# Kernel optimization log

Hardware: AMD Instinct MI355X
Metric: run time of the kernel (lower is better)

## Reference

```python
import jax, jax.numpy as jnp
import numpy as np

BLOCK_LEN = 64

def _segsum(x):
    """x: (..., T) -> (..., T, T) with segment sums on/below diagonal, -inf above."""
    T = x.shape[-1]
    cs = jnp.cumsum(x, axis=-1)
    seg = cs[..., :, None] - cs[..., None, :]
    mask = jnp.tril(jnp.ones((T, T), dtype=bool))
    return jnp.where(mask, seg, -jnp.inf)

def setup_inputs() -> dict:
    key = jax.random.key(0)
    kX, kA, kB, kC = jax.random.split(key, 4)
    B, S, H, P, N = 2, 4096, 32, 64, 64
    X = jax.random.normal(kX, (B, S, H, P), dtype=jnp.float32)
    # negative decay rates keep exp(cumsum) bounded (real Mamba2 uses A<0)
    A = -jnp.abs(jax.random.normal(kA, (B, S, H), dtype=jnp.float32)) * 0.1
    Bm = jax.random.normal(kB, (B, S, H, N), dtype=jnp.float32)
    Cm = jax.random.normal(kC, (B, S, H, N), dtype=jnp.float32)
    return {"X": X, "A": A, "Bm": Bm, "Cm": Cm}

def reference(X, A, Bm, Cm):
    b, s, h, p = X.shape
    n = Bm.shape[-1]
    l = BLOCK_LEN
    c = s // l
    Xb = X.reshape(b, c, l, h, p)
    Bb = Bm.reshape(b, c, l, h, n)
    Cb = Cm.reshape(b, c, l, h, n)
    Ab = A.reshape(b, c, l, h).transpose(0, 3, 1, 2)  # (b,h,c,l)

    # intra-chunk decay matrix L = exp(segsum(A))  (b,h,c,l,l)
    L = jnp.exp(_segsum(Ab))
    Y_diag = jnp.einsum('bclhn,bcshn,bhcls,bcshp->bclhp', Cb, Bb, L, Xb)

    A_cumsum = jnp.cumsum(Ab, axis=-1)  # (b,h,c,l)
    decay_states = jnp.exp(A_cumsum[..., :, -1:] - A_cumsum)
    states = jnp.einsum('bclhn,bhcl,bclhp->bchpn', Bb, decay_states, Xb)

    init = jnp.zeros_like(states[:, :1])
    states = jnp.concatenate([init, states], axis=1)  # (b,c+1,h,p,n)

    chunk_last = jnp.pad(A_cumsum[..., -1], ((0, 0), (0, 0), (1, 0)))  # (b,h,c+1)
    decay_chunk = jnp.exp(_segsum(chunk_last))  # (b,h,c+1,c+1)
    new_states = jnp.einsum('bhzc,bchpn->bzhpn', decay_chunk, states)
    states = new_states[:, :-1]  # (b,c,h,p,n)

    state_decay_out = jnp.exp(A_cumsum)
    Y_off = jnp.einsum('bclhn,bchpn,bhcl->bclhp', Cb, states, state_decay_out)

    Y = (Y_diag + Y_off).reshape(b, s, h, p)
    return Y
```

## Files before the change

kernel.cpp:

```cpp
#include <hip/hip_runtime.h>

#define B_ 2
#define S_ 4096
#define H_ 32
#define P_ 64
#define N_ 64
#define C_ 64
#define HP 2048
#define HN 2048

typedef __attribute__((ext_vector_type(8))) short bf16x8;
typedef __attribute__((ext_vector_type(4))) float f32x4;

__device__ __forceinline__ float bf2f(unsigned int u16) {
    return __uint_as_float(u16 << 16);
}
__device__ __forceinline__ void unpack2(unsigned int u, float& lo, float& hi) {
    lo = __uint_as_float(u << 16);
    hi = __uint_as_float(u & 0xffff0000u);
}
__device__ __forceinline__ unsigned short f2bf(float f) {
    unsigned int u = __float_as_uint(f);
    u += 0x7fffu + ((u >> 16) & 1u);
    return (unsigned short)(u >> 16);
}
__device__ __forceinline__ void split_bf(float x, unsigned short& h, unsigned short& l) {
    h = f2bf(x);
    l = f2bf(x - bf2f(h));
}

__device__ __forceinline__ int nsw(int r, int cb) {
    return (r << 7) + (cb ^ ((r & 7) << 4));
}
__device__ __forceinline__ int tsw(int r, int cb) {
    return (r << 7) + (cb ^ ((((r & 7) ^ (r >> 3)) & 7) << 4));
}

__global__ void k0_detect(const unsigned short* __restrict__ Au, int* __restrict__ flag)
{
    int tid = threadIdx.x;
    unsigned short u = Au[tid * 2];
    int positive = ((u & 0x8000u) == 0) ? 1 : 0;
    unsigned long long m = __ballot(positive);
    if (tid == 0) *flag = (__popcll(m) > 8) ? 1 : 0;
}

__global__ __launch_bounds__(256, 4) void k1u(
    const void* __restrict__ Xg,
    const void* __restrict__ Ag,
    const void* __restrict__ Bg,
    float* __restrict__ states,
    float* __restrict__ sums,
    const int* __restrict__ flag)
{
    __shared__ __align__(16) unsigned short XTh[4096];
    __shared__ __align__(16) unsigned short XTl[4096];
    __shared__ __align__(16) unsigned short BTh[4096];
    __shared__ __align__(16) unsigned short BTl[4096];
    __shared__ float wdec[64];

    const int tid = threadIdx.x;
    const int bid = blockIdx.x;
    const int h = bid & 31, c = (bid >> 5) & 63, b = bid >> 11;
    const int isf32 = *flag;

    if (tid < 64) {
        int ai = (b * S_ + c * 64 + tid) * H_ + h;
        float a = isf32 ? ((const float*)Ag)[ai] : bf2f(((const unsigned short*)Ag)[ai]);
        float x = a;
        #pragma unroll
        for (int off = 1; off < 64; off <<= 1) {
            float y = __shfl_up(x, off, 64);
            if (tid >= off) x += y;
        }
        float tot = __shfl(x, 63, 64);
        wdec[tid] = __expf(tot - x);
        if (tid == 63) sums[(b * H_ + h) * C_ + c] = tot;
    }
    __syncthreads();

    const size_t baseX = (size_t)((b * S_ + c * 64) * H_ + h) * P_;
    const size_t baseB = (size_t)((b * S_ + c * 64) * H_ + h) * N_;
    char* XThb = (char*)XTh;
    char* XTlb = (char*)XTl;
    char* BThb = (char*)BTh;
    char* BTlb = (char*)BTl;

    #pragma unroll
    for (int it = 0; it < 2; ++it) {
        int t = (tid >> 3) + it * 32;
        int e = (tid & 7) * 8;
        float xv[8], bv[8];
        if (isf32) {
            const float* Xp = (const float*)Xg + baseX + (size_t)t * HP + e;
            const float* Bp = (const float*)Bg + baseB + (size_t)t * HN + e;
            float4 x0 = *(const float4*)Xp;
            float4 x1 = *(const float4*)(Xp + 4);
            float4 b0 = *(const float4*)Bp;
            float4 b1 = *(const float4*)(Bp + 4);
            xv[0]=x0.x; xv[1]=x0.y; xv[2]=x0.z; xv[3]=x0.w;
            xv[4]=x1.x; xv[5]=x1.y; xv[6]=x1.z; xv[7]=x1.w;
            bv[0]=b0.x; bv[1]=b0.y; bv[2]=b0.z; bv[3]=b0.w;
            bv[4]=b1.x; bv[5]=b1.y; bv[6]=b1.z; bv[7]=b1.w;
        } else {
            const unsigned short* Xp = (const unsigned short*)Xg + baseX + (size_t)t * HP + e;
            const unsigned short* Bp = (const unsigned short*)Bg + baseB + (size_t)t * HN + e;
            uint4 rx = *(const uint4*)Xp;
            uint4 rb = *(const uint4*)Bp;
            unpack2(rx.x, xv[0], xv[1]); unpack2(rx.y, xv[2], xv[3]);
            unpack2(rx.z, xv[4], xv[5]); unpack2(rx.w, xv[6], xv[7]);
            unpack2(rb.x, bv[0], bv[1]); unpack2(rb.y, bv[2], bv[3]);
            unpack2(rb.z, bv[4], bv[5]); unpack2(rb.w, bv[6], bv[7]);
        }
        float w = wdec[t];
        #pragma unroll
        for (int i = 0; i < 8; ++i) {
            int o = tsw(e + i, 2 * t);
            unsigned short hh, ll;
            split_bf(xv[i], hh, ll);
            *(unsigned short*)(XThb + o) = hh;
            *(unsigned short*)(XTlb + o) = ll;
            split_bf(bv[i] * w, hh, ll);
            *(unsigned short*)(BThb + o) = hh;
            *(unsigned short*)(BTlb + o) = ll;
        }
    }
    __syncthreads();

    const int l = tid & 63, w4 = tid >> 6;
    const int lr = l & 15, q = l >> 4;
    const int rowA = 16 * w4 + lr;

    const int oa0 = tsw(rowA, 16 * q);
    const int oa1 = tsw(rowA, 16 * q + 64);
    bf16x8 a0h = *(const bf16x8*)(XThb + oa0);
    bf16x8 a1h = *(const bf16x8*)(XThb + oa1);
    bf16x8 a0l = *(const bf16x8*)(XTlb + oa0);
    bf16x8 a1l = *(const bf16x8*)(XTlb + oa1);

    f32x4 acc[4];
    #pragma unroll
    for (int nt = 0; nt < 4; ++nt) acc[nt] = (f32x4){0.f, 0.f, 0.f, 0.f};
    #pragma unroll
    for (int nt = 0; nt < 4; ++nt) {
        int ob0 = tsw(16 * nt + lr, 16 * q);
        int ob1 = tsw(16 * nt + lr, 16 * q + 64);
        bf16x8 b0h = *(const bf16x8*)(BThb + ob0);
        bf16x8 b0l = *(const bf16x8*)(BTlb + ob0);
        bf16x8 b1h = *(const bf16x8*)(BThb + ob1);
        bf16x8 b1l = *(const bf16x8*)(BTlb + ob1);
        acc[nt] = __builtin_amdgcn_mfma_f32_16x16x32_bf16(a0h, b0h, acc[nt], 0, 0, 0);
        acc[nt] = __builtin_amdgcn_mfma_f32_16x16x32_bf16(a1h, b1h, acc[nt], 0, 0, 0);
        acc[nt] = __builtin_amdgcn_mfma_f32_16x16x32_bf16(a0h, b0l, acc[nt], 0, 0, 0);
        acc[nt] = __builtin_amdgcn_mfma_f32_16x16x32_bf16(a1h, b1l, acc[nt], 0, 0, 0);
        acc[nt] = __builtin_amdgcn_mfma_f32_16x16x32_bf16(a0l, b0h, acc[nt], 0, 0, 0);
        acc[nt] = __builtin_amdgcn_mfma_f32_16x16x32_bf16(a1l, b1h, acc[nt], 0, 0, 0);
    }

    float* sp = states + (size_t)((b * C_ + c) * H_ + h) * 4096;
    #pragma unroll
    for (int nt = 0; nt < 4; ++nt)
        #pragma unroll
        for (int r = 0; r < 4; ++r) {
            int p = 16 * w4 + 4 * q + r;
            int n = 16 * nt + lr;
            sp[p * 64 + n] = acc[nt][r];
        }
}

__global__ __launch_bounds__(256) void k2_scan(
    float* __restrict__ states, const float* __restrict__ sums)
{
    const int tid = threadIdx.x;
    const int bid = blockIdx.x;
    const int split = bid & 7;
    const int bh = bid >> 3;
    const int h = bh & 31;
    const int b = bh >> 5;
    const int e = split * 512 + tid * 2;
    const float* sm = sums + (b * H_ + h) * C_;
    const size_t cstride = (size_t)H_ * 4096;
    float* p = states + ((size_t)(b * C_) * H_ + h) * 4096 + e;
    float2 S = make_float2(0.f, 0.f);
    float2 st = *(const float2*)p;
    #pragma unroll 4
    for (int c = 0; c < 64; ++c) {
        float2 stn = make_float2(0.f, 0.f);
        if (c < 63) stn = *(const float2*)(p + cstride);
        float d = __expf(sm[c]);
        *(float2*)p = S;
        S.x = S.x * d + st.x;
        S.y = S.y * d + st.y;
        st = stn;
        p += cstride;
    }
}

__global__ __launch_bounds__(256, 3) void k3u(
    const void* __restrict__ Xg,
    const void* __restrict__ Ag,
    const void* __restrict__ Bg,
    const void* __restrict__ Cg,
    const float* __restrict__ states,
    void* __restrict__ Yg,
    const int* __restrict__ flag)
{
    __shared__ __align__(16) unsigned short Ch[4096];
    __shared__ __align__(16) unsigned short Cl[4096];
    __shared__ __align__(16) unsigned short Bh[4096];
    __shared__ __align__(16) unsigned short Bl[4096];
    __shared__ __align__(16) unsigned short Sh[4096];
    __shared__ __align__(16) unsigned short Sl[4096];
    __shared__ float csh[64];

    const int tid = threadIdx.x;
    const int bid = blockIdx.x;
    const int h = bid & 31, c = (bid >> 5) & 63, b = bid >> 11;
    const int isf32 = *flag;

    if (tid < 64) {
        int ai = (b * S_ + c * 64 + tid) * H_ + h;
        float a = isf32 ? ((const float*)Ag)[ai] : bf2f(((const unsigned short*)Ag)[ai]);
        float x = a;
        #pragma unroll
        for (int off = 1; off < 64; off <<= 1) {
            float y = __shfl_up(x, off, 64);
            if (tid >= off) x += y;
        }
        csh[tid] = x;
    }

    const size_t baseX = (size_t)((b * S_ + c * 64) * H_ + h) * P_;
    const size_t baseN = (size_t)((b * S_ + c * 64) * H_ + h) * N_;
    char* Chb = (char*)Ch; char* Clb = (char*)Cl;
    char* Bhb = (char*)Bh; char* Blb = (char*)Bl;
    char* Shb = (char*)Sh; char* Slb = (char*)Sl;

    uint4 xq0[2], xq1[2];
    #pragma unroll
    for (int it = 0; it < 2; ++it) {
        int t = (tid >> 3) + it * 32;
        int e = (tid & 7) * 8;
        if (isf32) {
            const float* Xp = (const float*)Xg + baseX + (size_t)t * HP + e;
            xq0[it] = *(const uint4*)Xp;
            xq1[it] = *(const uint4*)(Xp + 4);
        } else {
            const unsigned short* Xp = (const unsigned short*)Xg + baseX + (size_t)t * HP + e;
            xq0[it] = *(const uint4*)Xp;
        }
    }

    #pragma unroll
    for (int it = 0; it < 2; ++it) {
        int t = (tid >> 3) + it * 32;
        int e = (tid & 7) * 8;
        float cv[8], bv[8];
        if (isf32) {
            const float* Cp = (const float*)Cg + baseN + (size_t)t * HN + e;
            const float* Bp = (const float*)Bg + baseN + (size_t)t * HN + e;
            float4 c0 = *(const float4*)Cp;
            float4 c1 = *(const float4*)(Cp + 4);
            float4 b0 = *(const float4*)Bp;
            float4 b1 = *(const float4*)(Bp + 4);
            cv[0]=c0.x; cv[1]=c0.y; cv[2]=c0.z; cv[3]=c0.w;
            cv[4]=c1.x; cv[5]=c1.y; cv[6]=c1.z; cv[7]=c1.w;
            bv[0]=b0.x; bv[1]=b0.y; bv[2]=b0.z; bv[3]=b0.w;
            bv[4]=b1.x; bv[5]=b1.y; bv[6]=b1.z; bv[7]=b1.w;
        } else {
            const unsigned short* Cp = (const unsigned short*)Cg + baseN + (size_t)t * HN + e;
            const unsigned short* Bp = (const unsigned short*)Bg + baseN + (size_t)t * HN + e;
            uint4 rc = *(const uint4*)Cp;
            uint4 rb = *(const uint4*)Bp;
            unpack2(rc.x, cv[0], cv[1]); unpack2(rc.y, cv[2], cv[3]);
            unpack2(rc.z, cv[4], cv[5]); unpack2(rc.w, cv[6], cv[7]);
            unpack2(rb.x, bv[0], bv[1]); unpack2(rb.y, bv[2], bv[3]);
            unpack2(rb.z, bv[4], bv[5]); unpack2(rb.w, bv[6], bv[7]);
        }
        int o = nsw(t, 2 * e);
        unsigned short hs[8], ls[8];
        #pragma unroll
        for (int i = 0; i < 8; ++i) split_bf(cv[i], hs[i], ls[i]);
        {
            uint4 uh, ul;
            uh.x = (unsigned int)hs[0] | ((unsigned int)hs[1] << 16);
            uh.y = (unsigned int)hs[2] | ((unsigned int)hs[3] << 16);
            uh.z = (unsigned int)hs[4] | ((unsigned int)hs[5] << 16);
            uh.w = (unsigned int)hs[6] | ((unsigned int)hs[7] << 16);
            ul.x = (unsigned int)ls[0] | ((unsigned int)ls[1] << 16);
            ul.y = (unsigned int)ls[2] | ((unsigned int)ls[3] << 16);
            ul.z = (unsigned int)ls[4] | ((unsigned int)ls[5] << 16);
            ul.w = (unsigned int)ls[6] | ((unsigned int)ls[7] << 16);
            *(uint4*)(Chb + o) = uh;
            *(uint4*)(Clb + o) = ul;
        }
        #pragma unroll
        for (int i = 0; i < 8; ++i) split_bf(bv[i], hs[i], ls[i]);
        {
            uint4 uh, ul;
            uh.x = (unsigned int)hs[0] | ((unsigned int)hs[1] << 16);
            uh.y = (unsigned int)hs[2] | ((unsigned int)hs[3] << 16);
            uh.z = (unsigned int)hs[4] | ((unsigned int)hs[5] << 16);
            uh.w = (unsigned int)hs[6] | ((unsigned int)hs[7] << 16);
            ul.x = (unsigned int)ls[0] | ((unsigned int)ls[1] << 16);
            ul.y = (unsigned int)ls[2] | ((unsigned int)ls[3] << 16);
            ul.z = (unsigned int)ls[4] | ((unsigned int)ls[5] << 16);
            ul.w = (unsigned int)ls[6] | ((unsigned int)ls[7] << 16);
            *(uint4*)(Bhb + o) = uh;
            *(uint4*)(Blb + o) = ul;
        }
    }

    {
        const float* sb = states + (size_t)((b * C_ + c) * H_ + h) * 4096;
        #pragma unroll
        for (int k = 0; k < 4; ++k) {
            int e2 = (k * 256 + tid) * 4;
            float4 v = *(const float4*)(sb + e2);
            unsigned short h0,l0,h1,l1,h2,l2,h3,l3;
            split_bf(v.x, h0, l0); split_bf(v.y, h1, l1);
            split_bf(v.z, h2, l2); split_bf(v.w, h3, l3);
            uint2 uh, ul;
            uh.x = (unsigned int)h0 | ((unsigned int)h1 << 16);
            uh.y = (unsigned int)h2 | ((unsigned int)h3 << 16);
            ul.x = (unsigned int)l0 | ((unsigned int)l1 << 16);
            ul.y = (unsigned int)l2 | ((unsigned int)l3 << 16);
            int o = nsw(e2 >> 6, 2 * (e2 & 63));
            *(uint2*)(Shb + o) = uh;
            *(uint2*)(Slb + o) = ul;
        }
    }
    __syncthreads();

    const int l = tid & 63, w4 = tid >> 6;
    const int lr = l & 15, q = l >> 4;
    const int tA = 16 * w4 + lr;

    const int oa0 = nsw(tA, 16 * q);
    const int oa1 = nsw(tA, 16 * q + 64);
    bf16x8 ac0h = *(const bf16x8*)(Chb + oa0);
    bf16x8 ac1h = *(const bf16x8*)(Chb + oa1);
    bf16x8 ac0l = *(const bf16x8*)(Clb + oa0);
    bf16x8 ac1l = *(const bf16x8*)(Clb + oa1);

    f32x4 mac[4];
    #pragma unroll
    for (int st = 0; st < 4; ++st) mac[st] = (f32x4){0.f, 0.f, 0.f, 0.f};
    #pragma unroll
    for (int st = 0; st < 4; ++st) {
        int ob0 = nsw(16 * st + lr, 16 * q);
        int ob1 = nsw(16 * st + lr, 16 * q + 64);
        bf16x8 b0h = *(const bf16x8*)(Bhb + ob0);
        bf16x8 b0l = *(const bf16x8*)(Blb + ob0);
        bf16x8 b1h = *(const bf16x8*)(Bhb + ob1);
        bf16x8 b1l = *(const bf16x8*)(Blb + ob1);
        mac[st] = __builtin_amdgcn_mfma_f32_16x16x32_bf16(ac0h, b0h, mac[st], 0, 0, 0);
        mac[st] = __builtin_amdgcn_mfma_f32_16x16x32_bf16(ac1h, b1h, mac[st], 0, 0, 0);
        mac[st] = __builtin_amdgcn_mfma_f32_16x16x32_bf16(ac0h, b0l, mac[st], 0, 0, 0);
        mac[st] = __builtin_amdgcn_mfma_f32_16x16x32_bf16(ac1h, b1l, mac[st], 0, 0, 0);
        mac[st] = __builtin_amdgcn_mfma_f32_16x16x32_bf16(ac0l, b0h, mac[st], 0, 0, 0);
        mac[st] = __builtin_amdgcn_mfma_f32_16x16x32_bf16(ac1l, b1h, mac[st], 0, 0, 0);
    }

    f32x4 yacO[4];
    #pragma unroll
    for (int pt = 0; pt < 4; ++pt) yacO[pt] = (f32x4){0.f, 0.f, 0.f, 0.f};
    #pragma unroll
    for (int pt = 0; pt < 4; ++pt) {
        int os0 = nsw(16 * pt + lr, 16 * q);
        int os1 = nsw(16 * pt + lr, 16 * q + 64);
        bf16x8 s0h = *(const bf16x8*)(Shb + os0);
        bf16x8 s0l = *(const bf16x8*)(Slb + os0);
        bf16x8 s1h = *(const bf16x8*)(Shb + os1);
        bf16x8 s1l = *(const bf16x8*)(Slb + os1);
        yacO[pt] = __builtin_amdgcn_mfma_f32_16x16x32_bf16(ac0h, s0h, yacO[pt], 0, 0, 0);
        yacO[pt] = __builtin_amdgcn_mfma_f32_16x16x32_bf16(ac1h, s1h, yacO[pt], 0, 0, 0);
        yacO[pt] = __builtin_amdgcn_mfma_f32_16x16x32_bf16(ac0h, s0l, yacO[pt], 0, 0, 0);
        yacO[pt] = __builtin_amdgcn_mfma_f32_16x16x32_bf16(ac1h, s1l, yacO[pt], 0, 0, 0);
        yacO[pt] = __builtin_amdgcn_mfma_f32_16x16x32_bf16(ac0l, s0h, yacO[pt], 0, 0, 0);
        yacO[pt] = __builtin_amdgcn_mfma_f32_16x16x32_bf16(ac1l, s1h, yacO[pt], 0, 0, 0);
    }
    __syncthreads();

    float ct[4];
    #pragma unroll
    for (int r = 0; r < 4; ++r) ct[r] = csh[16 * w4 + 4 * q + r];
    #pragma unroll
    for (int st = 0; st < 4; ++st) {
        int s = 16 * st + lr;
        float cs_s = csh[s];
        #pragma unroll
        for (int r = 0; r < 4; ++r) {
            int t = 16 * w4 + 4 * q + r;
            float v = (s <= t) ? mac[st][r] * __expf(ct[r] - cs_s) : 0.f;
            unsigned short hh, ll;
            split_bf(v, hh, ll);
            int o = nsw(t, 2 * s);
            *(unsigned short*)(Bhb + o) = hh;
            *(unsigned short*)(Blb + o) = ll;
        }
    }

    #pragma unroll
    for (int it = 0; it < 2; ++it) {
        int t = (tid >> 3) + it * 32;
        int e = (tid & 7) * 8;
        float xv[8];
        if (isf32) {
            xv[0] = __uint_as_float(xq0[it].x); xv[1] = __uint_as_float(xq0[it].y);
            xv[2] = __uint_as_float(xq0[it].z); xv[3] = __uint_as_float(xq0[it].w);
            xv[4] = __uint_as_float(xq1[it].x); xv[5] = __uint_as_float(xq1[it].y);
            xv[6] = __uint_as_float(xq1[it].z); xv[7] = __uint_as_float(xq1[it].w);
        } else {
            unpack2(xq0[it].x, xv[0], xv[1]); unpack2(xq0[it].y, xv[2], xv[3]);
            unpack2(xq0[it].z, xv[4], xv[5]); unpack2(xq0[it].w, xv[6], xv[7]);
        }
        #pragma unroll
        for (int i = 0; i < 8; ++i) {
            unsigned short hh, ll;
            split_bf(xv[i], hh, ll);
            int o = tsw(e + i, 2 * t);
            *(unsigned short*)(Shb + o) = hh;
            *(unsigned short*)(Slb + o) = ll;
        }
    }
    __syncthreads();

    const int om0 = nsw(tA, 16 * q);
    const int om1 = nsw(tA, 16 * q + 64);
    bf16x8 am0h = *(const bf16x8*)(Bhb + om0);
    bf16x8 am1h = *(const bf16x8*)(Bhb + om1);
    bf16x8 am0l = *(const bf16x8*)(Blb + om0);
    bf16x8 am1l = *(const bf16x8*)(Blb + om1);
    f32x4 yacD[4];
    #pragma unroll
    for (int pt = 0; pt < 4; ++pt) yacD[pt] = (f32x4){0.f, 0.f, 0.f, 0.f};
    #pragma unroll
    for (int pt = 0; pt < 4; ++pt) {
        int ox0 = tsw(16 * pt + lr, 16 * q);
        int ox1 = tsw(16 * pt + lr, 16 * q + 64);
        bf16x8 x0h = *(const bf16x8*)(Shb + ox0);
        bf16x8 x0l = *(const bf16x8*)(Slb + ox0);
        bf16x8 x1h = *(const bf16x8*)(Shb + ox1);
        bf16x8 x1l = *(const bf16x8*)(Slb + ox1);
        yacD[pt] = __builtin_amdgcn_mfma_f32_16x16x32_bf16(am0h, x0h, yacD[pt], 0, 0, 0);
        yacD[pt] = __builtin_amdgcn_mfma_f32_16x16x32_bf16(am1h, x1h, yacD[pt], 0, 0, 0);
        yacD[pt] = __builtin_amdgcn_mfma_f32_16x16x32_bf16(am0h, x0l, yacD[pt], 0, 0, 0);
        yacD[pt] = __builtin_amdgcn_mfma_f32_16x16x32_bf16(am1h, x1l, yacD[pt], 0, 0, 0);
        yacD[pt] = __builtin_amdgcn_mfma_f32_16x16x32_bf16(am0l, x0h, yacD[pt], 0, 0, 0);
        yacD[pt] = __builtin_amdgcn_mfma_f32_16x16x32_bf16(am1l, x1h, yacD[pt], 0, 0, 0);
    }

    float ge[4];
    #pragma unroll
    for (int r = 0; r < 4; ++r) ge[r] = __expf(ct[r]);
    if (!isf32) {
        unsigned short* Yp = (unsigned short*)Yg + baseX;
        #pragma unroll
        for (int pt = 0; pt < 4; ++pt)
            #pragma unroll
            for (int r = 0; r < 4; ++r) {
                int t = 16 * w4 + 4 * q + r;
                Yp[(size_t)t * HP + 16 * pt + lr] = f2bf(yacD[pt][r] + ge[r] * yacO[pt][r]);
            }
    } else {
        float* Yp = (float*)Yg + baseX;
        #pragma unroll
        for (int pt = 0; pt < 4; ++pt)
            #pragma unroll
            for (int r = 0; r < 4; ++r) {
                int t = 16 * w4 + 4 * q + r;
                Yp[(size_t)t * HP + 16 * pt + lr] = yacD[pt][r] + ge[r] * yacO[pt][r];
            }
    }
}

extern "C" void kernel_launch(void* const* d_in, const int* in_sizes, int n_in,
                              void* d_out, int out_size, void* d_ws, size_t ws_size,
                              hipStream_t stream) {
    const void* X  = d_in[0];
    const void* A  = d_in[1];
    const void* Bm = d_in[2];
    const void* Cm = d_in[3];

    int*   flag   = (int*)d_ws;
    float* sums   = (float*)d_ws + 16;
    float* states = (float*)d_ws + 16 + 4096;

    k0_detect<<<dim3(1), dim3(64), 0, stream>>>((const unsigned short*)A, flag);
    k1u<<<dim3(B_ * C_ * H_), dim3(256), 0, stream>>>(X, A, Bm, states, sums, flag);
    k2_scan<<<dim3(B_ * H_ * 8), dim3(256), 0, stream>>>(states, sums);
    k3u<<<dim3(B_ * C_ * H_), dim3(256), 0, stream>>>(X, A, Bm, Cm, states, d_out, flag);
}
```

Measured before the change: 282.6 us.

## Fuse detect, chunk-state, scan and output kernels into one cooperative persistent kernel

Replaces the four separate launches (dtype detect, per-chunk state GEMM, inter-chunk scan, output GEMM) with one cooperative kernel. Persistent blocks loop over tiles and are separated by grid-wide syncs. Loads are issued earlier so they overlap the decay scan, and the scan stage caches the per-chunk exp decays in shared memory and prefetches several chunks ahead. The aim is to remove launch gaps and per-kernel ramp costs. In exchange it adds grid.sync overhead and depends on the assumed count of 256 CUs and the occupancy query to size the grid.

```diff
diff --git a/kernel.cpp b/kernel.cpp
--- a/kernel.cpp
+++ b/kernel.cpp
@@ -1,4 +1,7 @@
 #include <hip/hip_runtime.h>
+#include <hip/hip_cooperative_groups.h>
+
+namespace cg = cooperative_groups;
 
 #define B_ 2
 #define S_ 4096
@@ -8,6 +11,7 @@
 #define C_ 64
 #define HP 2048
 #define HN 2048
+#define NTILE 4096
 
 typedef __attribute__((ext_vector_type(8))) short bf16x8;
 typedef __attribute__((ext_vector_type(4))) float f32x4;
@@ -36,459 +40,468 @@
     return (r << 7) + (cb ^ ((((r & 7) ^ (r >> 3)) & 7) << 4));
 }
 
-__global__ void k0_detect(const unsigned short* __restrict__ Au, int* __restrict__ flag)
-{
-    int tid = threadIdx.x;
-    unsigned short u = Au[tid * 2];
-    int positive = ((u & 0x8000u) == 0) ? 1 : 0;
-    unsigned long long m = __ballot(positive);
-    if (tid == 0) *flag = (__popcll(m) > 8) ? 1 : 0;
-}
-
-__global__ __launch_bounds__(256, 4) void k1u(
-    const void* __restrict__ Xg,
-    const void* __restrict__ Ag,
-    const void* __restrict__ Bg,
-    float* __restrict__ states,
-    float* __restrict__ sums,
-    const int* __restrict__ flag)
-{
-    __shared__ __align__(16) unsigned short XTh[4096];
-    __shared__ __align__(16) unsigned short XTl[4096];
-    __shared__ __align__(16) unsigned short BTh[4096];
-    __shared__ __align__(16) unsigned short BTl[4096];
-    __shared__ float wdec[64];
-
-    const int tid = threadIdx.x;
-    const int bid = blockIdx.x;
-    const int h = bid & 31, c = (bid >> 5) & 63, b = bid >> 11;
-    const int isf32 = *flag;
-
-    if (tid < 64) {
-        int ai = (b * S_ + c * 64 + tid) * H_ + h;
-        float a = isf32 ? ((const float*)Ag)[ai] : bf2f(((const unsigned short*)Ag)[ai]);
-        float x = a;
-        #pragma unroll
-        for (int off = 1; off < 64; off <<= 1) {
-            float y = __shfl_up(x, off, 64);
-            if (tid >= off) x += y;
-        }
-        float tot = __shfl(x, 63, 64);
-        wdec[tid] = __expf(tot - x);
-        if (tid == 63) sums[(b * H_ + h) * C_ + c] = tot;
-    }
-    __syncthreads();
-
-    const size_t baseX = (size_t)((b * S_ + c * 64) * H_ + h) * P_;
-    const size_t baseB = (size_t)((b * S_ + c * 64) * H_ + h) * N_;
-    char* XThb = (char*)XTh;
-    char* XTlb = (char*)XTl;
-    char* BThb = (char*)BTh;
-    char* BTlb = (char*)BTl;
-
-    #pragma unroll
-    for (int it = 0; it < 2; ++it) {
-        int t = (tid >> 3) + it * 32;
-        int e = (tid & 7) * 8;
-        float xv[8], bv[8];
-        if (isf32) {
-            const float* Xp = (const float*)Xg + baseX + (size_t)t * HP + e;
-            const float* Bp = (const float*)Bg + baseB + (size_t)t * HN + e;
-            float4 x0 = *(const float4*)Xp;
-            float4 x1 = *(const float4*)(Xp + 4);
-            float4 b0 = *(const float4*)Bp;
-            float4 b1 = *(const float4*)(Bp + 4);
-            xv[0]=x0.x; xv[1]=x0.y; xv[2]=x0.z; xv[3]=x0.w;
-            xv[4]=x1.x; xv[5]=x1.y; xv[6]=x1.z; xv[7]=x1.w;
-            bv[0]=b0.x; bv[1]=b0.y; bv[2]=b0.z; bv[3]=b0.w;
-            bv[4]=b1.x; bv[5]=b1.y; bv[6]=b1.z; bv[7]=b1.w;
-        } else {
-            const unsigned short* Xp = (const unsigned short*)Xg + baseX + (size_t)t * HP + e;
-            const unsigned short* Bp = (const unsigned short*)Bg + baseB + (size_t)t * HN + e;
-            uint4 rx = *(const uint4*)Xp;
-            uint4 rb = *(const uint4*)Bp;
-            unpack2(rx.x, xv[0], xv[1]); unpack2(rx.y, xv[2], xv[3]);
-            unpack2(rx.z, xv[4], xv[5]); unpack2(rx.w, xv[6], xv[7]);
-            unpack2(rb.x, bv[0], bv[1]); unpack2(rb.y, bv[2], bv[3]);
-            unpack2(rb.z, bv[4], bv[5]); unpack2(rb.w, bv[6], bv[7]);
-        }
-        float w = wdec[t];
-        #pragma unroll
-        for (int i = 0; i < 8; ++i) {
-            int o = tsw(e + i, 2 * t);
-            unsigned short hh, ll;
-            split_bf(xv[i], hh, ll);
-            *(unsigned short*)(XThb + o) = hh;
-            *(unsigned short*)(XTlb + o) = ll;
-            split_bf(bv[i] * w, hh, ll);
-            *(unsigned short*)(BThb + o) = hh;
-            *(unsigned short*)(BTlb + o) = ll;
-        }
-    }
-    __syncthreads();
-
-    const int l = tid & 63, w4 = tid >> 6;
-    const int lr = l & 15, q = l >> 4;
-    const int rowA = 16 * w4 + lr;
-
-    const int oa0 = tsw(rowA, 16 * q);
-    const int oa1 = tsw(rowA, 16 * q + 64);
-    bf16x8 a0h = *(const bf16x8*)(XThb + oa0);
-    bf16x8 a1h = *(const bf16x8*)(XThb + oa1);
-    bf16x8 a0l = *(const bf16x8*)(XTlb + oa0);
-    bf16x8 a1l = *(const bf16x8*)(XTlb + oa1);
-
-    f32x4 acc[4];
-    #pragma unroll
-    for (int nt = 0; nt < 4; ++nt) acc[nt] = (f32x4){0.f, 0.f, 0.f, 0.f};
-    #pragma unroll
-    for (int nt = 0; nt < 4; ++nt) {
-        int ob0 = tsw(16 * nt + lr, 16 * q);
-        int ob1 = tsw(16 * nt + lr, 16 * q + 64);
-        bf16x8 b0h = *(const bf16x8*)(BThb + ob0);
-        bf16x8 b0l = *(const bf16x8*)(BTlb + ob0);
-        bf16x8 b1h = *(const bf16x8*)(BThb + ob1);
-        bf16x8 b1l = *(const bf16x8*)(BTlb + ob1);
-        acc[nt] = __builtin_amdgcn_mfma_f32_16x16x32_bf16(a0h, b0h, acc[nt], 0, 0, 0);
-        acc[nt] = __builtin_amdgcn_mfma_f32_16x16x32_bf16(a1h, b1h, acc[nt], 0, 0, 0);
-        acc[nt] = __builtin_amdgcn_mfma_f32_16x16x32_bf16(a0h, b0l, acc[nt], 0, 0, 0);
-        acc[nt] = __builtin_amdgcn_mfma_f32_16x16x32_bf16(a1h, b1l, acc[nt], 0, 0, 0);
-        acc[nt] = __builtin_amdgcn_mfma_f32_16x16x32_bf16(a0l, b0h, acc[nt], 0, 0, 0);
-        acc[nt] = __builtin_amdgcn_mfma_f32_16x16x32_bf16(a1l, b1h, acc[nt], 0, 0, 0);
-    }
-
-    float* sp = states + (size_t)((b * C_ + c) * H_ + h) * 4096;
-    #pragma unroll
-    for (int nt = 0; nt < 4; ++nt)
-        #pragma unroll
-        for (int r = 0; r < 4; ++r) {
-            int p = 16 * w4 + 4 * q + r;
-            int n = 16 * nt + lr;
-            sp[p * 64 + n] = acc[nt][r];
-        }
-}
-
-__global__ __launch_bounds__(256) void k2_scan(
-    float* __restrict__ states, const float* __restrict__ sums)
-{
-    const int tid = threadIdx.x;
-    const int bid = blockIdx.x;
-    const int split = bid & 7;
-    const int bh = bid >> 3;
-    const int h = bh & 31;
-    const int b = bh >> 5;
-    const int e = split * 512 + tid * 2;
-    const float* sm = sums + (b * H_ + h) * C_;
-    const size_t cstride = (size_t)H_ * 4096;
-    float* p = states + ((size_t)(b * C_) * H_ + h) * 4096 + e;
-    float2 S = make_float2(0.f, 0.f);
-    float2 st = *(const float2*)p;
-    #pragma unroll 4
-    for (int c = 0; c < 64; ++c) {
-        float2 stn = make_float2(0.f, 0.f);
-        if (c < 63) stn = *(const float2*)(p + cstride);
-        float d = __expf(sm[c]);
-        *(float2*)p = S;
-        S.x = S.x * d + st.x;
-        S.y = S.y * d + st.y;
-        st = stn;
-        p += cstride;
-    }
-}
-
-__global__ __launch_bounds__(256, 3) void k3u(
+__global__ __launch_bounds__(256, 3) void fused(
     const void* __restrict__ Xg,
     const void* __restrict__ Ag,
     const void* __restrict__ Bg,
     const void* __restrict__ Cg,
-    const float* __restrict__ states,
-    void* __restrict__ Yg,
-    const int* __restrict__ flag)
+    float* __restrict__ states,
+    float* __restrict__ sums,
+    void* __restrict__ Yg)
 {
-    __shared__ __align__(16) unsigned short Ch[4096];
-    __shared__ __align__(16) unsigned short Cl[4096];
-    __shared__ __align__(16) unsigned short Bh[4096];
-    __shared__ __align__(16) unsigned short Bl[4096];
-    __shared__ __align__(16) unsigned short Sh[4096];
-    __shared__ __align__(16) unsigned short Sl[4096];
-    __shared__ float csh[64];
-
-    const int tid = threadIdx.x;
-    const int bid = blockIdx.x;
-    const int h = bid & 31, c = (bid >> 5) & 63, b = bid >> 11;
-    const int isf32 = *flag;
-
-    if (tid < 64) {
-        int ai = (b * S_ + c * 64 + tid) * H_ + h;
-        float a = isf32 ? ((const float*)Ag)[ai] : bf2f(((const unsigned short*)Ag)[ai]);
-        float x = a;
-        #pragma unroll
-        for (int off = 1; off < 64; off <<= 1) {
-            float y = __shfl_up(x, off, 64);
-            if (tid >= off) x += y;
-        }
-        csh[tid] = x;
+    __shared__ __align__(16) unsigned char pool[49408];
+    char*  p0  = (char*)pool;
+    float* fsh = (float*)(pool + 49152);
+
+    const int tid  = threadIdx.x;
+    const int nblk = gridDim.x;
+    cg::grid_group grid = cg::this_grid();
+
+    int isf32;
+    {
+        unsigned short du = ((const unsigned short*)Ag)[(tid & 63) * 2];
+        unsigned long long m = __ballot(((du & 0x8000u) == 0) ? 1 : 0);
+        isf32 = (__popcll(m) > 8) ? 1 : 0;
     }
 
-    const size_t baseX = (size_t)((b * S_ + c * 64) * H_ + h) * P_;
-    const size_t baseN = (size_t)((b * S_ + c * 64) * H_ + h) * N_;
-    char* Chb = (char*)Ch; char* Clb = (char*)Cl;
-    char* Bhb = (char*)Bh; char* Blb = (char*)Bl;
-    char* Shb = (char*)Sh; char* Slb = (char*)Sl;
-
-    uint4 xq0[2], xq1[2];
-    #pragma unroll
-    for (int it = 0; it < 2; ++it) {
-        int t = (tid >> 3) + it * 32;
-        int e = (tid & 7) * 8;
-        if (isf32) {
-            const float* Xp = (const float*)Xg + baseX + (size_t)t * HP + e;
-            xq0[it] = *(const uint4*)Xp;
-            xq1[it] = *(const uint4*)(Xp + 4);
-        } else {
-            const unsigned short* Xp = (const unsigned short*)Xg + baseX + (size_t)t * HP + e;
-            xq0[it] = *(const uint4*)Xp;
-        }
+    const int l  = tid & 63, w4 = tid >> 6;
+    const int lr = l & 15,  q  = l >> 4;
+
+    for (int tile = blockIdx.x; tile < NTILE; tile += nblk) {
+        const int h = tile & 31, c = (tile >> 5) & 63, b = tile >> 11;
+        char* XThb = p0;
+        char* XTlb = p0 + 8192;
+        char* BThb = p0 + 16384;
+        char* BTlb = p0 + 24576;
+        float* wdec = fsh;
+
+        const size_t baseX = (size_t)((b * S_ + c * 64) * H_ + h) * P_;
+        const size_t baseB = (size_t)((b * S_ + c * 64) * H_ + h) * N_;
+
+        uint4 xA[2], xB[2], bA[2], bB[2];
+        #pragma unroll
+        for (int it = 0; it < 2; ++it) {
+            int t = (tid >> 3) + it * 32;
+            int e = (tid & 7) * 8;
+            if (isf32) {
+                const float* Xp = (const float*)Xg + baseX + (size_t)t * HP + e;
+                const float* Bp = (const float*)Bg + baseB + (size_t)t * HN + e;
+                xA[it] = *(const uint4*)Xp;
+                xB[it] = *(const uint4*)(Xp + 4);
+                bA[it] = *(const uint4*)Bp;
+                bB[it] = *(const uint4*)(Bp + 4);
+            } else {
+                const unsigned short* Xp = (const unsigned short*)Xg + baseX + (size_t)t * HP + e;
+                const unsigned short* Bp = (const unsigned short*)Bg + baseB + (size_t)t * HN + e;
+                xA[it] = *(const uint4*)Xp;
+                bA[it] = *(const uint4*)Bp;
+            }
+        }
+
+        if (tid < 64) {
+            int ai = (b * S_ + c * 64 + tid) * H_ + h;
+            float a = isf32 ? ((const float*)Ag)[ai] : bf2f(((const unsigned short*)Ag)[ai]);
+            float x = a;
+            #pragma unroll
+            for (int off = 1; off < 64; off <<= 1) {
+                float y = __shfl_up(x, off, 64);
+                if (tid >= off) x += y;
+            }
+            float tot = __shfl(x, 63, 64);
+            wdec[tid] = __expf(tot - x);
+            if (tid == 63) sums[(b * H_ + h) * C_ + c] = tot;
+        }
+        __syncthreads();
+
+        #pragma unroll
+        for (int it = 0; it < 2; ++it) {
+            int t = (tid >> 3) + it * 32;
+            int e = (tid & 7) * 8;
+            float xv[8], bv[8];
+            if (isf32) {
+                xv[0]=__uint_as_float(xA[it].x); xv[1]=__uint_as_float(xA[it].y);
+                xv[2]=__uint_as_float(xA[it].z); xv[3]=__uint_as_float(xA[it].w);
+                xv[4]=__uint_as_float(xB[it].x); xv[5]=__uint_as_float(xB[it].y);
+                xv[6]=__uint_as_float(xB[it].z); xv[7]=__uint_as_float(xB[it].w);
+                bv[0]=__uint_as_float(bA[it].x); bv[1]=__uint_as_float(bA[it].y);
+                bv[2]=__uint_as_float(bA[it].z); bv[3]=__uint_as_float(bA[it].w);
+                bv[4]=__uint_as_float(bB[it].x); bv[5]=__uint_as_float(bB[it].y);
+                bv[6]=__uint_as_float(bB[it].z); bv[7]=__uint_as_float(bB[it].w);
+            } else {
+                unpack2(xA[it].x, xv[0], xv[1]); unpack2(xA[it].y, xv[2], xv[3]);
+                unpack2(xA[it].z, xv[4], xv[5]); unpack2(xA[it].w, xv[6], xv[7]);
+                unpack2(bA[it].x, bv[0], bv[1]); unpack2(bA[it].y, bv[2], bv[3]);
+                unpack2(bA[it].z, bv[4], bv[5]); unpack2(bA[it].w, bv[6], bv[7]);
+            }
+            float w = wdec[t];
+            #pragma unroll
+            for (int i = 0; i < 8; ++i) {
+                int o = tsw(e + i, 2 * t);
+                unsigned short hh, ll;
+                split_bf(xv[i], hh, ll);
+                *(unsigned short*)(XThb + o) = hh;
+                *(unsigned short*)(XTlb + o) = ll;
+                split_bf(bv[i] * w, hh, ll);
+                *(unsigned short*)(BThb + o) = hh;
+                *(unsigned short*)(BTlb + o) = ll;
+            }
+        }
+        __syncthreads();
+
+        const int rowA = 16 * w4 + lr;
+        const int oa0 = tsw(rowA, 16 * q);
+        const int oa1 = tsw(rowA, 16 * q + 64);
+        bf16x8 a0h = *(const bf16x8*)(XThb + oa0);
+        bf16x8 a1h = *(const bf16x8*)(XThb + oa1);
+        bf16x8 a0l = *(const bf16x8*)(XTlb + oa0);
+        bf16x8 a1l = *(const bf16x8*)(XTlb + oa1);
+
+        f32x4 acc[4];
+        #pragma unroll
+        for (int nt = 0; nt < 4; ++nt) acc[nt] = (f32x4){0.f, 0.f, 0.f, 0.f};
+        #pragma unroll
+        for (int nt = 0; nt < 4; ++nt) {
+            int ob0 = tsw(16 * nt + lr, 16 * q);
+            int ob1 = tsw(16 * nt + lr, 16 * q + 64);
+            bf16x8 b0h = *(const bf16x8*)(BThb + ob0);
+            bf16x8 b0l = *(const bf16x8*)(BTlb + ob0);
+            bf16x8 b1h = *(const bf16x8*)(BThb + ob1);
+            bf16x8 b1l = *(const bf16x8*)(BTlb + ob1);
+            acc[nt] = __builtin_amdgcn_mfma_f32_16x16x32_bf16(a0h, b0h, acc[nt], 0, 0, 0);
+            acc[nt] = __builtin_amdgcn_mfma_f32_16x16x32_bf16(a1h, b1h, acc[nt], 0, 0, 0);
+            acc[nt] = __builtin_amdgcn_mfma_f32_16x16x32_bf16(a0h, b0l, acc[nt], 0, 0, 0);
+            acc[nt] = __builtin_amdgcn_mfma_f32_16x16x32_bf16(a1h, b1l, acc[nt], 0, 0, 0);
+            acc[nt] = __builtin_amdgcn_mfma_f32_16x16x32_bf16(a0l, b0h, acc[nt], 0, 0, 0);
+            acc[nt] = __builtin_amdgcn_mfma_f32_16x16x32_bf16(a1l, b1h, acc[nt], 0, 0, 0);
+        }
+
+        float* sp = states + (size_t)((b * C_ + c) * H_ + h) * 4096;
+        #pragma unroll
+        for (int nt = 0; nt < 4; ++nt)
+            #pragma unroll
+            for (int r = 0; r < 4; ++r) {
+                int p = 16 * w4 + 4 * q + r;
+                int n = 16 * nt + lr;
+                sp[p * 64 + n] = acc[nt][r];
+            }
+        __syncthreads();
     }
 
-    #pragma unroll
-    for (int it = 0; it < 2; ++it) {
-        int t = (tid >> 3) + it * 32;
-        int e = (tid & 7) * 8;
-        float cv[8], bv[8];
-        if (isf32) {
-            const float* Cp = (const float*)Cg + baseN + (size_t)t * HN + e;
-            const float* Bp = (const float*)Bg + baseN + (size_t)t * HN + e;
-            float4 c0 = *(const float4*)Cp;
-            float4 c1 = *(const float4*)(Cp + 4);
-            float4 b0 = *(const float4*)Bp;
-            float4 b1 = *(const float4*)(Bp + 4);
-            cv[0]=c0.x; cv[1]=c0.y; cv[2]=c0.z; cv[3]=c0.w;
-            cv[4]=c1.x; cv[5]=c1.y; cv[6]=c1.z; cv[7]=c1.w;
-            bv[0]=b0.x; bv[1]=b0.y; bv[2]=b0.z; bv[3]=b0.w;
-            bv[4]=b1.x; bv[5]=b1.y; bv[6]=b1.z; bv[7]=b1.w;
-        } else {
-            const unsigned short* Cp = (const unsigned short*)Cg + baseN + (size_t)t * HN + e;
-            const unsigned short* Bp = (const unsigned short*)Bg + baseN + (size_t)t * HN + e;
-            uint4 rc = *(const uint4*)Cp;
-            uint4 rb = *(const uint4*)Bp;
-            unpack2(rc.x, cv[0], cv[1]); unpack2(rc.y, cv[2], cv[3]);
-            unpack2(rc.z, cv[4], cv[5]); unpack2(rc.w, cv[6], cv[7]);
-            unpack2(rb.x, bv[0], bv[1]); unpack2(rb.y, bv[2], bv[3]);
-            unpack2(rb.z, bv[4], bv[5]); unpack2(rb.w, bv[6], bv[7]);
-        }
-        int o = nsw(t, 2 * e);
-        unsigned short hs[8], ls[8];
-        #pragma unroll
-        for (int i = 0; i < 8; ++i) split_bf(cv[i], hs[i], ls[i]);
+    grid.sync();
+
+    for (int u = blockIdx.x; u < 512; u += nblk) {
+        const int split = u & 7;
+        const int bh = u >> 3;
+        const int h = bh & 31;
+        const int b = bh >> 5;
+        __syncthreads();
+        if (tid < 64) fsh[tid] = __expf(sums[(b * H_ + h) * C_ + tid]);
+        __syncthreads();
+        const int e = split * 512 + tid * 2;
+        float* p = states + ((size_t)(b * C_) * H_ + h) * 4096 + e;
+        const size_t cstr = (size_t)H_ * 4096;
+        float2 S = make_float2(0.f, 0.f);
+        float2 buf[4];
+        #pragma unroll
+        for (int d = 0; d < 4; ++d) buf[d] = *(const float2*)(p + d * cstr);
+        #pragma unroll 4
+        for (int cc = 0; cc < 64; ++cc) {
+            float2 st = buf[cc & 3];
+            if (cc + 4 < 64) buf[cc & 3] = *(const float2*)(p + (size_t)(cc + 4) * cstr);
+            float dg = fsh[cc];
+            *(float2*)(p + (size_t)cc * cstr) = S;
+            S.x = S.x * dg + st.x;
+            S.y = S.y * dg + st.y;
+        }
+    }
+
+    grid.sync();
+
+    for (int tile = blockIdx.x; tile < NTILE; tile += nblk) {
+        const int h = tile & 31, c = (tile >> 5) & 63, b = tile >> 11;
+        char* Chb = p0;
+        char* Clb = p0 + 8192;
+        char* Bhb = p0 + 16384;
+        char* Blb = p0 + 24576;
+        char* Shb = p0 + 32768;
+        char* Slb = p0 + 40960;
+        float* csh = fsh;
+
+        if (tid < 64) {
+            int ai = (b * S_ + c * 64 + tid) * H_ + h;
+            float a = isf32 ? ((const float*)Ag)[ai] : bf2f(((const unsigned short*)Ag)[ai]);
+            float x = a;
+            #pragma unroll
+            for (int off = 1; off < 64; off <<= 1) {
+                float y = __shfl_up(x, off, 64);
+                if (tid >= off) x += y;
+            }
+            csh[tid] = x;
+        }
+
+        const size_t baseX = (size_t)((b * S_ + c * 64) * H_ + h) * P_;
+        const size_t baseN = (size_t)((b * S_ + c * 64) * H_ + h) * N_;
+
+        uint4 xq0[2], xq1[2];
+        #pragma unroll
+        for (int it = 0; it < 2; ++it) {
+            int t = (tid >> 3) + it * 32;
+            int e = (tid & 7) * 8;
+            if (isf32) {
+                const float* Xp = (const float*)Xg + baseX + (size_t)t * HP + e;
+                xq0[it] = *(const uint4*)Xp;
+                xq1[it] = *(const uint4*)(Xp + 4);
+            } else {
+                const unsigned short* Xp = (const unsigned short*)Xg + baseX + (size_t)t * HP + e;
+                xq0[it] = *(const uint4*)Xp;
+            }
+        }
+
+        #pragma unroll
+        for (int it = 0; it < 2; ++it) {
+            int t = (tid >> 3) + it * 32;
+            int e = (tid & 7) * 8;
+            float cv[8], bv[8];
+            if (isf32) {
+                const float* Cp = (const float*)Cg + baseN + (size_t)t * HN + e;
+                const float* Bp = (const float*)Bg + baseN + (size_t)t * HN + e;
+                float4 c0 = *(const float4*)Cp;
+                float4 c1 = *(const float4*)(Cp + 4);
+                float4 b0 = *(const float4*)Bp;
+                float4 b1 = *(const float4*)(Bp + 4);
+                cv[0]=c0.x; cv[1]=c0.y; cv[2]=c0.z; cv[3]=c0.w;
+                cv[4]=c1.x; cv[5]=c1.y; cv[6]=c1.z; cv[7]=c1.w;
+                bv[0]=b0.x; bv[1]=b0.y; bv[2]=b0.z; bv[3]=b0.w;
+                bv[4]=b1.x; bv[5]=b1.y; bv[6]=b1.z; bv[7]=b1.w;
+            } else {
+                const unsigned short* Cp = (const unsigned short*)Cg + baseN + (size_t)t * HN + e;
+                const unsigned short* Bp = (const unsigned short*)Bg + baseN + (size_t)t * HN + e;
+                uint4 rc = *(const uint4*)Cp;
+                uint4 rb = *(const uint4*)Bp;
+                unpack2(rc.x, cv[0], cv[1]); unpack2(rc.y, cv[2], cv[3]);
+                unpack2(rc.z, cv[4], cv[5]); unpack2(rc.w, cv[6], cv[7]);
+                unpack2(rb.x, bv[0], bv[1]); unpack2(rb.y, bv[2], bv[3]);
+                unpack2(rb.z, bv[4], bv[5]); unpack2(rb.w, bv[6], bv[7]);
+            }
+            int o = nsw(t, 2 * e);
+            unsigned short hs[8], ls[8];
+            #pragma unroll
+            for (int i = 0; i < 8; ++i) split_bf(cv[i], hs[i], ls[i]);
+            {
+                uint4 uh, ul;
+                uh.x = (unsigned int)hs[0] | ((unsigned int)hs[1] << 16);
+                uh.y = (unsigned int)hs[2] | ((unsigned int)hs[3] << 16);
+                uh.z = (unsigned int)hs[4] | ((unsigned int)hs[5] << 16);
+                uh.w = (unsigned int)hs[6] | ((unsigned int)hs[7] << 16);
+                ul.x = (unsigned int)ls[0] | ((unsigned int)ls[1] << 16);
+                ul.y = (unsigned int)ls[2] | ((unsigned int)ls[3] << 16);
+                ul.z = (unsigned int)ls[4] | ((unsigned int)ls[5] << 16);
+                ul.w = (unsigned int)ls[6] | ((unsigned int)ls[7] << 16);
+                *(uint4*)(Chb + o) = uh;
+                *(uint4*)(Clb + o) = ul;
+            }
+            #pragma unroll
+            for (int i = 0; i < 8; ++i) split_bf(bv[i], hs[i], ls[i]);
+            {
+                uint4 uh, ul;
+                uh.x = (unsigned int)hs[0] | ((unsigned int)hs[1] << 16);
+                uh.y = (unsigned int)hs[2] | ((unsigned int)hs[3] << 16);
+                uh.z = (unsigned int)hs[4] | ((unsigned int)hs[5] << 16);
+                uh.w = (unsigned int)hs[6] | ((unsigned int)hs[7] << 16);
+                ul.x = (unsigned int)ls[0] | ((unsigned int)ls[1] << 16);
+                ul.y = (unsigned int)ls[2] | ((unsigned int)ls[3] << 16);
+                ul.z = (unsigned int)ls[4] | ((unsigned int)ls[5] << 16);
+                ul.w = (unsigned int)ls[6] | ((unsigned int)ls[7] << 16);
+                *(uint4*)(Bhb + o) = uh;
+                *(uint4*)(Blb + o) = ul;
+            }
+        }
+
         {
-            uint4 uh, ul;
-            uh.x = (unsigned int)hs[0] | ((unsigned int)hs[1] << 16);
-            uh.y = (unsigned int)hs[2] | ((unsigned int)hs[3] << 16);
-            uh.z = (unsigned int)hs[4] | ((unsigned int)hs[5] << 16);
-            uh.w = (unsigned int)hs[6] | ((unsigned int)hs[7] << 16);
-            ul.x = (unsigned int)ls[0] | ((unsigned int)ls[1] << 16);
-            ul.y = (unsigned int)ls[2] | ((unsigned int)ls[3] << 16);
-            ul.z = (unsigned int)ls[4] | ((unsigned int)ls[5] << 16);
-            ul.w = (unsigned int)ls[6] | ((unsigned int)ls[7] << 16);
-            *(uint4*)(Chb + o) = uh;
-            *(uint4*)(Clb + o) = ul;
-        }
-        #pragma unroll
-        for (int i = 0; i < 8; ++i) split_bf(bv[i], hs[i], ls[i]);
-        {
-            uint4 uh, ul;
-            uh.x = (unsigned int)hs[0] | ((unsigned int)hs[1] << 16);
-            uh.y = (unsigned int)hs[2] | ((unsigned int)hs[3] << 16);
-            uh.z = (unsigned int)hs[4] | ((unsigned int)hs[5] << 16);
-            uh.w = (unsigned int)hs[6] | ((unsigned int)hs[7] << 16);
-            ul.x = (unsigned int)ls[0] | ((unsigned int)ls[1] << 16);
-            ul.y = (unsigned int)ls[2] | ((unsigned int)ls[3] << 16);
-            ul.z = (unsigned int)ls[4] | ((unsigned int)ls[5] << 16);
-            ul.w = (unsigned int)ls[6] | ((unsigned int)ls[7] << 16);
-            *(uint4*)(Bhb + o) = uh;
-            *(uint4*)(Blb + o) = ul;
-        }
-    }
-
-    {
-        const float* sb = states + (size_t)((b * C_ + c) * H_ + h) * 4096;
-        #pragma unroll
-        for (int k = 0; k < 4; ++k) {
-            int e2 = (k * 256 + tid) * 4;
-            float4 v = *(const float4*)(sb + e2);
-            unsigned short h0,l0,h1,l1,h2,l2,h3,l3;
-            split_bf(v.x, h0, l0); split_bf(v.y, h1, l1);
-            split_bf(v.z, h2, l2); split_bf(v.w, h3, l3);
-            uint2 uh, ul;
-            uh.x = (unsigned int)h0 | ((unsigned int)h1 << 16);
-            uh.y = (unsigned int)h2 | ((unsigned int)h3 << 16);
-            ul.x = (unsigned int)l0 | ((unsigned int)l1 << 16);
-            ul.y = (unsigned int)l2 | ((unsigned int)l3 << 16);
-            int o = nsw(e2 >> 6, 2 * (e2 & 63));
-            *(uint2*)(Shb + o) = uh;
-            *(uint2*)(Slb + o) = ul;
-        }
-    }
-    __syncthreads();
-
-    const int l = tid & 63, w4 = tid >> 6;
-    const int lr = l & 15, q = l >> 4;
-    const int tA = 16 * w4 + lr;
-
-    const int oa0 = nsw(tA, 16 * q);
-    const int oa1 = nsw(tA, 16 * q + 64);
-    bf16x8 ac0h = *(const bf16x8*)(Chb + oa0);
-    bf16x8 ac1h = *(const bf16x8*)(Chb + oa1);
-    bf16x8 ac0l = *(const bf16x8*)(Clb + oa0);
-    bf16x8 ac1l = *(const bf16x8*)(Clb + oa1);
-
-    f32x4 mac[4];
-    #pragma unroll
-    for (int st = 0; st < 4; ++st) mac[st] = (f32x4){0.f, 0.f, 0.f, 0.f};
-    #pragma unroll
-    for (int st = 0; st < 4; ++st) {
-        int ob0 = nsw(16 * st + lr, 16 * q);
-        int ob1 = nsw(16 * st + lr, 16 * q + 64);
-        bf16x8 b0h = *(const bf16x8*)(Bhb + ob0);
-        bf16x8 b0l = *(const bf16x8*)(Blb + ob0);
-        bf16x8 b1h = *(const bf16x8*)(Bhb + ob1);
-        bf16x8 b1l = *(const bf16x8*)(Blb + ob1);
-        mac[st] = __builtin_amdgcn_mfma_f32_16x16x32_bf16(ac0h, b0h, mac[st], 0, 0, 0);
-        mac[st] = __builtin_amdgcn_mfma_f32_16x16x32_bf16(ac1h, b1h, mac[st], 0, 0, 0);
-        mac[st] = __builtin_amdgcn_mfma_f32_16x16x32_bf16(ac0h, b0l, mac[st], 0, 0, 0);
-        mac[st] = __builtin_amdgcn_mfma_f32_16x16x32_bf16(ac1h, b1l, mac[st], 0, 0, 0);
-        mac[st] = __builtin_amdgcn_mfma_f32_16x16x32_bf16(ac0l, b0h, mac[st], 0, 0, 0);
-        mac[st] = __builtin_amdgcn_mfma_f32_16x16x32_bf16(ac1l, b1h, mac[st], 0, 0, 0);
-    }
-
-    f32x4 yacO[4];
-    #pragma unroll
-    for (int pt = 0; pt < 4; ++pt) yacO[pt] = (f32x4){0.f, 0.f, 0.f, 0.f};
-    #pragma unroll
-    for (int pt = 0; pt < 4; ++pt) {
-        int os0 = nsw(16 * pt + lr, 16 * q);
-        int os1 = nsw(16 * pt + lr, 16 * q + 64);
-        bf16x8 s0h = *(const bf16x8*)(Shb + os0);
-        bf16x8 s0l = *(const bf16x8*)(Slb + os0);
-        bf16x8 s1h = *(const bf16x8*)(Shb + os1);
-        bf16x8 s1l = *(const bf16x8*)(Slb + os1);
-        yacO[pt] = __builtin_amdgcn_mfma_f32_16x16x32_bf16(ac0h, s0h, yacO[pt], 0, 0, 0);
-        yacO[pt] = __builtin_amdgcn_mfma_f32_16x16x32_bf16(ac1h, s1h, yacO[pt], 0, 0, 0);
-        yacO[pt] = __builtin_amdgcn_mfma_f32_16x16x32_bf16(ac0h, s0l, yacO[pt], 0, 0, 0);
-        yacO[pt] = __builtin_amdgcn_mfma_f32_16x16x32_bf16(ac1h, s1l, yacO[pt], 0, 0, 0);
-        yacO[pt] = __builtin_amdgcn_mfma_f32_16x16x32_bf16(ac0l, s0h, yacO[pt], 0, 0, 0);
-        yacO[pt] = __builtin_amdgcn_mfma_f32_16x16x32_bf16(ac1l, s1h, yacO[pt], 0, 0, 0);
-    }
-    __syncthreads();
-
-    float ct[4];
-    #pragma unroll
-    for (int r = 0; r < 4; ++r) ct[r] = csh[16 * w4 + 4 * q + r];
-    #pragma unroll
-    for (int st = 0; st < 4; ++st) {
-        int s = 16 * st + lr;
-        float cs_s = csh[s];
-        #pragma unroll
-        for (int r = 0; r < 4; ++r) {
-            int t = 16 * w4 + 4 * q + r;
-            float v = (s <= t) ? mac[st][r] * __expf(ct[r] - cs_s) : 0.f;
-            unsigned short hh, ll;
-            split_bf(v, hh, ll);
-            int o = nsw(t, 2 * s);
-            *(unsigned short*)(Bhb + o) = hh;
-            *(unsigned short*)(Blb + o) = ll;
-        }
-    }
-
-    #pragma unroll
-    for (int it = 0; it < 2; ++it) {
-        int t = (tid >> 3) + it * 32;
-        int e = (tid & 7) * 8;
-        float xv[8];
-        if (isf32) {
-            xv[0] = __uint_as_float(xq0[it].x); xv[1] = __uint_as_float(xq0[it].y);
-            xv[2] = __uint_as_float(xq0[it].z); xv[3] = __uint_as_float(xq0[it].w);
-            xv[4] = __uint_as_float(xq1[it].x); xv[5] = __uint_as_float(xq1[it].y);
-            xv[6] = __uint_as_float(xq1[it].z); xv[7] = __uint_as_float(xq1[it].w);
-        } else {
-            unpack2(xq0[it].x, xv[0], xv[1]); unpack2(xq0[it].y, xv[2], xv[3]);
-            unpack2(xq0[it].z, xv[4], xv[5]); unpack2(xq0[it].w, xv[6], xv[7]);
-        }
-        #pragma unroll
-        for (int i = 0; i < 8; ++i) {
-            unsigned short hh, ll;
-            split_bf(xv[i], hh, ll);
-            int o = tsw(e + i, 2 * t);
-            *(unsigned short*)(Shb + o) = hh;
-            *(unsigned short*)(Slb + o) = ll;
-        }
-    }
-    __syncthreads();
-
-    const int om0 = nsw(tA, 16 * q);
-    const int om1 = nsw(tA, 16 * q + 64);
-    bf16x8 am0h = *(const bf16x8*)(Bhb + om0);
-    bf16x8 am1h = *(const bf16x8*)(Bhb + om1);
-    bf16x8 am0l = *(const bf16x8*)(Blb + om0);
-    bf16x8 am1l = *(const bf16x8*)(Blb + om1);
-    f32x4 yacD[4];
-    #pragma unroll
-    for (int pt = 0; pt < 4; ++pt) yacD[pt] = (f32x4){0.f, 0.f, 0.f, 0.f};
-    #pragma unroll
-    for (int pt = 0; pt < 4; ++pt) {
-        int ox0 = tsw(16 * pt + lr, 16 * q);
-        int ox1 = tsw(16 * pt + lr, 16 * q + 64);
-        bf16x8 x0h = *(const bf16x8*)(Shb + ox0);
-        bf16x8 x0l = *(const bf16x8*)(Slb + ox0);
-        bf16x8 x1h = *(const bf16x8*)(Shb + ox1);
-        bf16x8 x1l = *(const bf16x8*)(Slb + ox1);
-        yacD[pt] = __builtin_amdgcn_mfma_f32_16x16x32_bf16(am0h, x0h, yacD[pt], 0, 0, 0);
-        yacD[pt] = __builtin_amdgcn_mfma_f32_16x16x32_bf16(am1h, x1h, yacD[pt], 0, 0, 0);
-        yacD[pt] = __builtin_amdgcn_mfma_f32_16x16x32_bf16(am0h, x0l, yacD[pt], 0, 0, 0);
-        yacD[pt] = __builtin_amdgcn_mfma_f32_16x16x32_bf16(am1h, x1l, yacD[pt], 0, 0, 0);
-        yacD[pt] = __builtin_amdgcn_mfma_f32_16x16x32_bf16(am0l, x0h, yacD[pt], 0, 0, 0);
-        yacD[pt] = __builtin_amdgcn_mfma_f32_16x16x32_bf16(am1l, x1h, yacD[pt], 0, 0, 0);
-    }
-
-    float ge[4];
-    #pragma unroll
-    for (int r = 0; r < 4; ++r) ge[r] = __expf(ct[r]);
-    if (!isf32) {
-        unsigned short* Yp = (unsigned short*)Yg + baseX;
-        #pragma unroll
-        for (int pt = 0; pt < 4; ++pt)
+            const float* sb = states + (size_t)((b * C_ + c) * H_ + h) * 4096;
+            #pragma unroll
+            for (int k = 0; k < 4; ++k) {
+                int e2 = (k * 256 + tid) * 4;
+                float4 v = *(const float4*)(sb + e2);
+                unsigned short h0,l0,h1,l1,h2,l2,h3,l3;
+                split_bf(v.x, h0, l0); split_bf(v.y, h1, l1);
+                split_bf(v.z, h2, l2); split_bf(v.w, h3, l3);
+                uint2 uh, ul;
+                uh.x = (unsigned int)h0 | ((unsigned int)h1 << 16);
+                uh.y = (unsigned int)h2 | ((unsigned int)h3 << 16);
+                ul.x = (unsigned int)l0 | ((unsigned int)l1 << 16);
+                ul.y = (unsigned int)l2 | ((unsigned int)l3 << 16);
+                int o = nsw(e2 >> 6, 2 * (e2 & 63));
+                *(uint2*)(Shb + o) = uh;
+                *(uint2*)(Slb + o) = ul;
+            }
+        }
+        __syncthreads();
+
+        const int tA = 16 * w4 + lr;
+        const int oa0 = nsw(tA, 16 * q);
+        const int oa1 = nsw(tA, 16 * q + 64);
+        bf16x8 ac0h = *(const bf16x8*)(Chb + oa0);
+        bf16x8 ac1h = *(const bf16x8*)(Chb + oa1);
+        bf16x8 ac0l = *(const bf16x8*)(Clb + oa0);
+        bf16x8 ac1l = *(const bf16x8*)(Clb + oa1);
+
+        f32x4 mac[4];
+        #pragma unroll
+        for (int st = 0; st < 4; ++st) mac[st] = (f32x4){0.f, 0.f, 0.f, 0.f};
+        #pragma unroll
+        for (int st = 0; st < 4; ++st) {
+            int ob0 = nsw(16 * st + lr, 16 * q);
+            int ob1 = nsw(16 * st + lr, 16 * q + 64);
+            bf16x8 b0h = *(const bf16x8*)(Bhb + ob0);
+            bf16x8 b0l = *(const bf16x8*)(Blb + ob0);
+            bf16x8 b1h = *(const bf16x8*)(Bhb + ob1);
+            bf16x8 b1l = *(const bf16x8*)(Blb + ob1);
+            mac[st] = __builtin_amdgcn_mfma_f32_16x16x32_bf16(ac0h, b0h, mac[st], 0, 0, 0);
+            mac[st] = __builtin_amdgcn_mfma_f32_16x16x32_bf16(ac1h, b1h, mac[st], 0, 0, 0);
+            mac[st] = __builtin_amdgcn_mfma_f32_16x16x32_bf16(ac0h, b0l, mac[st], 0, 0, 0);
+            mac[st] = __builtin_amdgcn_mfma_f32_16x16x32_bf16(ac1h, b1l, mac[st], 0, 0, 0);
+            mac[st] = __builtin_amdgcn_mfma_f32_16x16x32_bf16(ac0l, b0h, mac[st], 0, 0, 0);
+            mac[st] = __builtin_amdgcn_mfma_f32_16x16x32_bf16(ac1l, b1h, mac[st], 0, 0, 0);
+        }
+
+        f32x4 yacO[4];
+        #pragma unroll
+        for (int pt = 0; pt < 4; ++pt) yacO[pt] = (f32x4){0.f, 0.f, 0.f, 0.f};
+        #pragma unroll
+        for (int pt = 0; pt < 4; ++pt) {
+            int os0 = nsw(16 * pt + lr, 16 * q);
+            int os1 = nsw(16 * pt + lr, 16 * q + 64);
+            bf16x8 s0h = *(const bf16x8*)(Shb + os0);
+            bf16x8 s0l = *(const bf16x8*)(Slb + os0);
+            bf16x8 s1h = *(const bf16x8*)(Shb + os1);
+            bf16x8 s1l = *(const bf16x8*)(Slb + os1);
+            yacO[pt] = __builtin_amdgcn_mfma_f32_16x16x32_bf16(ac0h, s0h, yacO[pt], 0, 0, 0);
+            yacO[pt] = __builtin_amdgcn_mfma_f32_16x16x32_bf16(ac1h, s1h, yacO[pt], 0, 0, 0);
+            yacO[pt] = __builtin_amdgcn_mfma_f32_16x16x32_bf16(ac0h, s0l, yacO[pt], 0, 0, 0);
+            yacO[pt] = __builtin_amdgcn_mfma_f32_16x16x32_bf16(ac1h, s1l, yacO[pt], 0, 0, 0);
+            yacO[pt] = __builtin_amdgcn_mfma_f32_16x16x32_bf16(ac0l, s0h, yacO[pt], 0, 0, 0);
+            yacO[pt] = __builtin_amdgcn_mfma_f32_16x16x32_bf16(ac1l, s1h, yacO[pt], 0, 0, 0);
+        }
+        __syncthreads();
+
+        float ct[4];
+        #pragma unroll
+        for (int r = 0; r < 4; ++r) ct[r] = csh[16 * w4 + 4 * q + r];
+        #pragma unroll
+        for (int st = 0; st < 4; ++st) {
+            int s = 16 * st + lr;
+            float cs_s = csh[s];
             #pragma unroll
             for (int r = 0; r < 4; ++r) {
                 int t = 16 * w4 + 4 * q + r;
-                Yp[(size_t)t * HP + 16 * pt + lr] = f2bf(yacD[pt][r] + ge[r] * yacO[pt][r]);
-            }
-    } else {
-        float* Yp = (float*)Yg + baseX;
-        #pragma unroll
-        for (int pt = 0; pt < 4; ++pt)
-            #pragma unroll
-            for (int r = 0; r < 4; ++r) {
-                int t = 16 * w4 + 4 * q + r;
-                Yp[(size_t)t * HP + 16 * pt + lr] = yacD[pt][r] + ge[r] * yacO[pt][r];
-            }
+                float v = (s <= t) ? mac[st][r] * __expf(ct[r] - cs_s) : 0.f;
+                unsigned short hh, ll;
+                split_bf(v, hh, ll);
+                int o = nsw(t, 2 * s);
+                *(unsigned short*)(Bhb + o) = hh;
+                *(unsigned short*)(Blb + o) = ll;
+            }
+        }
+
+        #pragma unroll
+        for (int it = 0; it < 2; ++it) {
+            int t = (tid >> 3) + it * 32;
+            int e = (tid & 7) * 8;
+            float xv[8];
+            if (isf32) {
+                xv[0] = __uint_as_float(xq0[it].x); xv[1] = __uint_as_float(xq0[it].y);
+                xv[2] = __uint_as_float(xq0[it].z); xv[3] = __uint_as_float(xq0[it].w);
+                xv[4] = __uint_as_float(xq1[it].x); xv[5] = __uint_as_float(xq1[it].y);
+                xv[6] = __uint_as_float(xq1[it].z); xv[7] = __uint_as_float(xq1[it].w);
+            } else {
+                unpack2(xq0[it].x, xv[0], xv[1]); unpack2(xq0[it].y, xv[2], xv[3]);
+                unpack2(xq0[it].z, xv[4], xv[5]); unpack2(xq0[it].w, xv[6], xv[7]);
+            }
+            #pragma unroll
+            for (int i = 0; i < 8; ++i) {
+                unsigned short hh, ll;
+                split_bf(xv[i], hh, ll);
+                int o = tsw(e + i, 2 * t);
+                *(unsigned short*)(Shb + o) = hh;
+                *(unsigned short*)(Slb + o) = ll;
+            }
+        }
+        __syncthreads();
+
+        const int om0 = nsw(tA, 16 * q);
+        const int om1 = nsw(tA, 16 * q + 64);
+        bf16x8 am0h = *(const bf16x8*)(Bhb + om0);
+        bf16x8 am1h = *(const bf16x8*)(Bhb + om1);
+        bf16x8 am0l = *(const bf16x8*)(Blb + om0);
+        bf16x8 am1l = *(const bf16x8*)(Blb + om1);
+        f32x4 yacD[4];
+        #pragma unroll
+        for (int pt = 0; pt < 4; ++pt) yacD[pt] = (f32x4){0.f, 0.f, 0.f, 0.f};
+        #pragma unroll
+        for (int pt = 0; pt < 4; ++pt) {
+            int ox0 = tsw(16 * pt + lr, 16 * q);
+            int ox1 = tsw(16 * pt + lr, 16 * q + 64);
+            bf16x8 x0h = *(const bf16x8*)(Shb + ox0);
+            bf16x8 x0l = *(const bf16x8*)(Slb + ox0);
+            bf16x8 x1h = *(const bf16x8*)(Shb + ox1);
+            bf16x8 x1l = *(const bf16x8*)(Slb + ox1);
+            yacD[pt] = __builtin_amdgcn_mfma_f32_16x16x32_bf16(am0h, x0h, yacD[pt], 0, 0, 0);
+            yacD[pt] = __builtin_amdgcn_mfma_f32_16x16x32_bf16(am1h, x1h, yacD[pt], 0, 0, 0);
+            yacD[pt] = __builtin_amdgcn_mfma_f32_16x16x32_bf16(am0h, x0l, yacD[pt], 0, 0, 0);
+            yacD[pt] = __builtin_amdgcn_mfma_f32_16x16x32_bf16(am1h, x1l, yacD[pt], 0, 0, 0);
+            yacD[pt] = __builtin_amdgcn_mfma_f32_16x16x32_bf16(am0l, x0h, yacD[pt], 0, 0, 0);
+            yacD[pt] = __builtin_amdgcn_mfma_f32_16x16x32_bf16(am1l, x1h, yacD[pt], 0, 0, 0);
+        }
+
+        float ge[4];
+        #pragma unroll
+        for (int r = 0; r < 4; ++r) ge[r] = __expf(ct[r]);
+        if (!isf32) {
+            unsigned short* Yp = (unsigned short*)Yg + baseX;
+            #pragma unroll
+            for (int pt = 0; pt < 4; ++pt)
+                #pragma unroll
+                for (int r = 0; r < 4; ++r) {
+                    int t = 16 * w4 + 4 * q + r;
+                    Yp[(size_t)t * HP + 16 * pt + lr] = f2bf(yacD[pt][r] + ge[r] * yacO[pt][r]);
+                }
+        } else {
+            float* Yp = (float*)Yg + baseX;
+            #pragma unroll
+            for (int pt = 0; pt < 4; ++pt)
+                #pragma unroll
+                for (int r = 0; r < 4; ++r) {
+                    int t = 16 * w4 + 4 * q + r;
+                    Yp[(size_t)t * HP + 16 * pt + lr] = yacD[pt][r] + ge[r] * yacO[pt][r];
+                }
+        }
+        __syncthreads();
     }
 }
 
 extern "C" void kernel_launch(void* const* d_in, const int* in_sizes, int n_in,
                               void* d_out, int out_size, void* d_ws, size_t ws_size,
                               hipStream_t stream) {
-    const void* X  = d_in[0];
-    const void* A  = d_in[1];
-    const void* Bm = d_in[2];
-    const void* Cm = d_in[3];
-
-    int*   flag   = (int*)d_ws;
+    void* X  = d_in[0];
+    void* A  = d_in[1];
+    void* Bm = d_in[2];
+    void* Cm = d_in[3];
+
     float* sums   = (float*)d_ws + 16;
     float* states = (float*)d_ws + 16 + 4096;
-
-    k0_detect<<<dim3(1), dim3(64), 0, stream>>>((const unsigned short*)A, flag);
-    k1u<<<dim3(B_ * C_ * H_), dim3(256), 0, stream>>>(X, A, Bm, states, sums, flag);
-    k2_scan<<<dim3(B_ * H_ * 8), dim3(256), 0, stream>>>(states, sums);
-    k3u<<<dim3(B_ * C_ * H_), dim3(256), 0, stream>>>(X, A, Bm, Cm, states, d_out, flag);
-}
+    void*  Y      = d_out;
+
+    static int grid_blocks = 0;
+    if (grid_blocks == 0) {
+        int nb = 0;
+        hipError_t e = hipOccupancyMaxActiveBlocksPerMultiprocessor(&nb, fused, 256, 0);
+        if (e != hipSuccess || nb < 1) nb = 1;
+        if (nb > 3) nb = 3;
+        grid_blocks = nb * 256;
+    }
+
+    void* args[] = { &X, &A, &Bm, &Cm, (void*)&states, (void*)&sums, &Y };
+    hipLaunchCooperativeKernel((const void*)fused, dim3(grid_blocks), dim3(256),
+                               args, 0, stream);
+}
```

After: 394.4 us. 1.4x slower.
